# Optimization experiments

Hardware: AMD Instinct MI355X
Metric: run time of the kernel (lower is better)

## Reference

```python
import jax, jax.numpy as jnp
import numpy as np

STATE_DIM = 512
ACTION_FEAT_DIM = 64
HIDDEN = 256


def setup_inputs() -> dict:
    key = jax.random.key(0)
    ks = jax.random.split(key, 8)
    B, K = 256, 1000
    state_embed = jax.random.normal(ks[0], (B, STATE_DIM), dtype=jnp.float32)
    action_feats = jax.random.normal(ks[1], (B, K, ACTION_FEAT_DIM), dtype=jnp.float32)
    s = 0.05
    W1 = jax.random.normal(ks[2], (STATE_DIM + ACTION_FEAT_DIM, HIDDEN), dtype=jnp.float32) * s
    b1 = jnp.zeros((HIDDEN,), dtype=jnp.float32)
    W2 = jax.random.normal(ks[3], (HIDDEN, HIDDEN // 2), dtype=jnp.float32) * s
    b2 = jnp.zeros((HIDDEN // 2,), dtype=jnp.float32)
    W3 = jax.random.normal(ks[4], (HIDDEN // 2, 1), dtype=jnp.float32) * s
    b3 = jnp.zeros((1,), dtype=jnp.float32)
    return {"state_embed": state_embed, "action_feats": action_feats,
            "W1": W1, "b1": b1, "W2": W2, "b2": b2, "W3": W3, "b3": b3}


def reference(state_embed, action_feats, W1, b1, W2, b2, W3, b3):
    # Faithful math: concat([state broadcast to K, action_feats]) -> Linear/ReLU x2 -> Linear(1)
    # Efficient form: split W1 rows so state part is computed once per batch row.
    W1_s = W1[:STATE_DIM]            # [state_dim, hidden]
    W1_a = W1[STATE_DIM:]            # [action_feat_dim, hidden]
    h_state = state_embed @ W1_s     # [B, hidden]
    h = jax.nn.relu(jnp.einsum('bkf,fh->bkh', action_feats, W1_a) + h_state[:, None, :] + b1)
    h = jax.nn.relu(jnp.einsum('bkh,hg->bkg', h, W2) + b2)
    logits = (jnp.einsum('bkg,go->bko', h, W3) + b3)[..., 0]  # [B, K]
    return logits
```

## Files before the change

kernel.cpp:

```cpp
#include <hip/hip_runtime.h>

typedef _Float16 f16;
typedef f16 f16x4 __attribute__((ext_vector_type(4)));
typedef f16 f16x8 __attribute__((ext_vector_type(8)));
typedef float f32x4 __attribute__((ext_vector_type(4)));


#define AF_STRIDE 64
#define H1_STRIDE 256

__global__ __launch_bounds__(256) void prep_kernel(const float* __restrict__ W1,
                                                   const float* __restrict__ W2,
                                                   const float* __restrict__ state,
                                                   const float* __restrict__ b1,
                                                   f16* __restrict__ pw1at,
                                                   f16* __restrict__ pw2,
                                                   float* __restrict__ hstate) {
    __shared__ float srow[512];
    int blk = blockIdx.x;
    int tid = threadIdx.x;
    if (blk < 24) {
        int idx = blk * 256 + tid;
        int F = idx >> 6;
        int L = idx & 63;
        int q = L >> 4, c = L & 15;
        f16x8 v;
        if (F < 32) {
            int mt = F >> 1, kt = F & 1;
            #pragma unroll
            for (int j = 0; j < 8; ++j) {
                int f = kt * 32 + q * 8 + j;
                v[j] = (f16)W1[(size_t)(512 + f) * 256 + mt * 16 + c];
            }
            *(f16x8*)(pw1at + ((size_t)F * 64 + L) * 8) = v;
        } else {
            int F2 = F - 32;
            int nt = F2 >> 3, kt = F2 & 7;
            #pragma unroll
            for (int j = 0; j < 8; ++j) {
                int k = kt * 32 + q * 8 + j;
                v[j] = (f16)W2[(size_t)k * 128 + nt * 16 + c];
            }
            *(f16x8*)(pw2 + ((size_t)F2 * 64 + L) * 8) = v;
        }
    } else {
        int b = blk - 24;
        srow[tid] = state[(size_t)b * 512 + tid];
        srow[tid + 256] = state[(size_t)b * 512 + 256 + tid];
        __syncthreads();
        float a0 = 0.f, a1 = 0.f;
        #pragma unroll 8
        for (int f = 0; f < 512; f += 2) {
            a0 = fmaf(srow[f],     W1[(size_t)f * 256 + tid],       a0);
            a1 = fmaf(srow[f + 1], W1[(size_t)(f + 1) * 256 + tid], a1);
        }
        hstate[(size_t)b * 256 + tid] = a0 + a1 + b1[tid];
    }
}

__global__ __launch_bounds__(256, 4) void fused_kernel(const float* __restrict__ afeat,
                                                       const float* __restrict__ hstate,
                                                       const f16* __restrict__ pw1at,
                                                       const f16* __restrict__ pw2,
                                                       const float* __restrict__ b2,
                                                       const float* __restrict__ W3,
                                                       const float* __restrict__ b3,
                                                       float* __restrict__ out) {
    __shared__ __align__(16) char smem[(64 * AF_STRIDE + 64 * H1_STRIDE) * 2];
    f16* afs = (f16*)smem;
    f16* h1s = (f16*)(smem + 64 * AF_STRIDE * 2);
    float* lds3 = (float*)smem;

    int tid = threadIdx.x;
    int w = tid >> 6;
    int L = tid & 63;
    int q = L >> 4, c = L & 15;
    int r0 = blockIdx.x * 64;

    f16x8 a1f[4][2];
    #pragma unroll
    for (int i = 0; i < 4; ++i)
        #pragma unroll
        for (int kt = 0; kt < 2; ++kt)
            a1f[i][kt] = *(const f16x8*)(pw1at + ((size_t)((4 * w + i) * 2 + kt) * 64 + L) * 8);

    #pragma unroll
    for (int i = 0; i < 2; ++i) {
        int id = i * 256 + tid;
        int row = id >> 3, c32 = id & 7;
        const float* p = afeat + (size_t)(r0 + row) * 64 + c32 * 8;
        f32x4 lo = *(const f32x4*)p;
        f32x4 hi = *(const f32x4*)(p + 4);
        f16x8 v;
        v[0] = (f16)lo[0]; v[1] = (f16)lo[1]; v[2] = (f16)lo[2]; v[3] = (f16)lo[3];
        v[4] = (f16)hi[0]; v[5] = (f16)hi[1]; v[6] = (f16)hi[2]; v[7] = (f16)hi[3];
        *(f16x8*)(afs + row * AF_STRIDE + ((c32 * 8) ^ ((row & 7) << 3))) = v;
    }

    float b3v = b3[0];
    float b2v[2], w3v[2];
    #pragma unroll
    for (int ntl = 0; ntl < 2; ++ntl) {
        int col = (w * 2 + ntl) * 16 + c;
        b2v[ntl] = b2[col];
        w3v[ntl] = W3[col];
    }
    __syncthreads();

    int b0i = r0 / 1000;
    int boundary = (b0i + 1) * 1000;
    int b1i = b0i < 255 ? b0i + 1 : 255;
    int sx = (c & 7) << 3;

    f16x8 bf[4][2];
    #pragma unroll
    for (int nt = 0; nt < 4; ++nt)
        #pragma unroll
        for (int kt = 0; kt < 2; ++kt)
            bf[nt][kt] = *(const f16x8*)(afs + (nt * 16 + c) * AF_STRIDE + ((kt * 32 + q * 8) ^ sx));

    #pragma unroll
    for (int i = 0; i < 4; ++i) {
        f32x4 acc[4];
        #pragma unroll
        for (int nt = 0; nt < 4; ++nt) {
            acc[nt] = (f32x4){0.f, 0.f, 0.f, 0.f};
            #pragma unroll
            for (int kt = 0; kt < 2; ++kt)
                acc[nt] = __builtin_amdgcn_mfma_f32_16x16x32_f16(
                    a1f[i][kt], bf[nt][kt], acc[nt], 0, 0, 0);
        }
        int hbase = (4 * w + i) * 16 + q * 4;
        f32x4 hsA = *(const f32x4*)(hstate + (size_t)b0i * 256 + hbase);
        f32x4 hsB = *(const f32x4*)(hstate + (size_t)b1i * 256 + hbase);
        #pragma unroll
        for (int nt = 0; nt < 4; ++nt) {
            bool sel = (r0 + nt * 16 + c) >= boundary;
            f16x4 hv;
            #pragma unroll
            for (int reg = 0; reg < 4; ++reg) {
                float v = acc[nt][reg] + (sel ? hsB[reg] : hsA[reg]);
                v = v > 0.f ? v : 0.f;
                hv[reg] = (f16)v;
            }
            *(f16x4*)(h1s + (nt * 16 + c) * H1_STRIDE + (hbase ^ sx)) = hv;
        }
    }
    __syncthreads();

    f32x4 acc2[4][2];
    #pragma unroll
    for (int rb = 0; rb < 4; ++rb) {
        acc2[rb][0] = (f32x4){0.f, 0.f, 0.f, 0.f};
        acc2[rb][1] = (f32x4){0.f, 0.f, 0.f, 0.f};
    }
    #pragma unroll
    for (int kt = 0; kt < 8; ++kt) {
        f16x8 a2[4];
        #pragma unroll
        for (int rb = 0; rb < 4; ++rb)
            a2[rb] = *(const f16x8*)(h1s + (rb * 16 + c) * H1_STRIDE + ((kt * 32 + q * 8) ^ sx));
        #pragma unroll
        for (int ntl = 0; ntl < 2; ++ntl) {
            f16x8 bfr = *(const f16x8*)(pw2 + ((size_t)((w * 2 + ntl) * 8 + kt) * 64 + L) * 8);
            #pragma unroll
            for (int rb = 0; rb < 4; ++rb)
                acc2[rb][ntl] = __builtin_amdgcn_mfma_f32_16x16x32_f16(
                    a2[rb], bfr, acc2[rb][ntl], 0, 0, 0);
        }
    }

    float p[16];
    #pragma unroll
    for (int rb = 0; rb < 4; ++rb)
        #pragma unroll
        for (int reg = 0; reg < 4; ++reg) {
            float v0 = acc2[rb][0][reg] + b2v[0]; v0 = v0 > 0.f ? v0 : 0.f;
            float v1 = acc2[rb][1][reg] + b2v[1]; v1 = v1 > 0.f ? v1 : 0.f;
            p[rb * 4 + reg] = fmaf(v0, w3v[0], v1 * w3v[1]);
        }
    float s0[8];
    #pragma unroll
    for (int i = 0; i < 8; ++i) {
        float send = (c & 1) ? p[2 * i] : p[2 * i + 1];
        float keep = (c & 1) ? p[2 * i + 1] : p[2 * i];
        s0[i] = keep + __shfl_xor(send, 1);
    }
    float s1[4];
    #pragma unroll
    for (int i = 0; i < 4; ++i) {
        float send = (c & 2) ? s0[2 * i] : s0[2 * i + 1];
        float keep = (c & 2) ? s0[2 * i + 1] : s0[2 * i];
        s1[i] = keep + __shfl_xor(send, 2);
    }
    float s2[2];
    #pragma unroll
    for (int i = 0; i < 2; ++i) {
        float send = (c & 4) ? s1[2 * i] : s1[2 * i + 1];
        float keep = (c & 4) ? s1[2 * i + 1] : s1[2 * i];
        s2[i] = keep + __shfl_xor(send, 4);
    }
    float send3 = (c & 8) ? s2[0] : s2[1];
    float keep3 = (c & 8) ? s2[1] : s2[0];
    float s3 = keep3 + __shfl_xor(send3, 8);
    int m = (c >> 2) * 16 + q * 4 + (c & 3);
    lds3[m * 6 + w] = s3;
    __syncthreads();

    if (tid < 64) {
        const float* pm = lds3 + tid * 6;
        out[r0 + tid] = pm[0] + pm[1] + pm[2] + pm[3] + b3v;
    }
}

extern "C" void kernel_launch(void* const* d_in, const int* in_sizes, int n_in,
                              void* d_out, int out_size, void* d_ws, size_t ws_size,
                              hipStream_t stream) {
    const float* state = (const float*)d_in[0];
    const float* afeat = (const float*)d_in[1];
    const float* W1    = (const float*)d_in[2];
    const float* b1    = (const float*)d_in[3];
    const float* W2    = (const float*)d_in[4];
    const float* b2    = (const float*)d_in[5];
    const float* W3    = (const float*)d_in[6];
    const float* b3    = (const float*)d_in[7];
    float* out = (float*)d_out;

    float* hstate = (float*)d_ws;
    f16* pw1at = (f16*)((char*)d_ws + 65536 * sizeof(float));
    f16* pw2   = pw1at + 16384;

    prep_kernel<<<280, 256, 0, stream>>>(W1, W2, state, b1, pw1at, pw2, hstate);
    fused_kernel<<<4000, 256, 0, stream>>>(afeat, hstate, pw1at, pw2, b2, W3, b3, out);
}
```

Before: 137.0 us.

## Swap layer-2 MFMA operands, prefetch W2 fragments, simplify logit reduction

Layer 2 now passes the W2 fragment as the A operand and the hidden activations as B, so each lane's accumulator holds four hidden columns for one row. This lets the W3 dot product run mostly in registers, followed by two cross-lane shuffles instead of a four-stage shuffle tree. W2 fragments are double-buffered one k-step ahead, hstate loads are hoisted before the layer-1 MFMAs, and the prep loop's unroll factor goes from 8 to 16. The aim is to hide global load latency and cut shuffle and ALU work in the epilogue, at the cost of more registers under the 4-blocks-per-CU launch bound.

```diff
diff --git a/kernel.cpp b/kernel.cpp
--- a/kernel.cpp
+++ b/kernel.cpp
@@ -49,7 +49,7 @@
         srow[tid + 256] = state[(size_t)b * 512 + 256 + tid];
         __syncthreads();
         float a0 = 0.f, a1 = 0.f;
-        #pragma unroll 8
+        #pragma unroll 16
         for (int f = 0; f < 512; f += 2) {
             a0 = fmaf(srow[f],     W1[(size_t)f * 256 + tid],       a0);
             a1 = fmaf(srow[f + 1], W1[(size_t)(f + 1) * 256 + tid], a1);
@@ -97,19 +97,21 @@
         *(f16x8*)(afs + row * AF_STRIDE + ((c32 * 8) ^ ((row & 7) << 3))) = v;
     }
 
-    float b3v = b3[0];
-    float b2v[2], w3v[2];
-    #pragma unroll
-    for (int ntl = 0; ntl < 2; ++ntl) {
-        int col = (w * 2 + ntl) * 16 + c;
-        b2v[ntl] = b2[col];
-        w3v[ntl] = W3[col];
-    }
-    __syncthreads();
-
     int b0i = r0 / 1000;
     int boundary = (b0i + 1) * 1000;
     int b1i = b0i < 255 ? b0i + 1 : 255;
+
+    f32x4 hsva[4], hsvb[4];
+    #pragma unroll
+    for (int i = 0; i < 4; ++i) {
+        int hbase = (4 * w + i) * 16 + q * 4;
+        hsva[i] = *(const f32x4*)(hstate + (size_t)b0i * 256 + hbase);
+        hsvb[i] = *(const f32x4*)(hstate + (size_t)b1i * 256 + hbase);
+    }
+
+    float b3v = b3[0];
+    __syncthreads();
+
     int sx = (c & 7) << 3;
 
     f16x8 bf[4][2];
@@ -131,15 +133,13 @@
                     a1f[i][kt], bf[nt][kt], acc[nt], 0, 0, 0);
         }
         int hbase = (4 * w + i) * 16 + q * 4;
-        f32x4 hsA = *(const f32x4*)(hstate + (size_t)b0i * 256 + hbase);
-        f32x4 hsB = *(const f32x4*)(hstate + (size_t)b1i * 256 + hbase);
         #pragma unroll
         for (int nt = 0; nt < 4; ++nt) {
             bool sel = (r0 + nt * 16 + c) >= boundary;
             f16x4 hv;
             #pragma unroll
             for (int reg = 0; reg < 4; ++reg) {
-                float v = acc[nt][reg] + (sel ? hsB[reg] : hsA[reg]);
+                float v = acc[nt][reg] + (sel ? hsvb[i][reg] : hsva[i][reg]);
                 v = v > 0.f ? v : 0.f;
                 hv[reg] = (f16)v;
             }
@@ -147,6 +147,14 @@
         }
     }
     __syncthreads();
+
+    f32x4 b2v[2], w3v[2];
+    #pragma unroll
+    for (int gti = 0; gti < 2; ++gti) {
+        int gb = (2 * w + gti) * 16 + q * 4;
+        b2v[gti] = *(const f32x4*)(b2 + gb);
+        w3v[gti] = *(const f32x4*)(W3 + gb);
+    }
 
     f32x4 acc2[4][2];
     #pragma unroll
@@ -154,57 +162,56 @@
         acc2[rb][0] = (f32x4){0.f, 0.f, 0.f, 0.f};
         acc2[rb][1] = (f32x4){0.f, 0.f, 0.f, 0.f};
     }
+
+    f16x8 pwf[2][2];
+    #pragma unroll
+    for (int gti = 0; gti < 2; ++gti)
+        pwf[0][gti] = *(const f16x8*)(pw2 + ((size_t)((2 * w + gti) * 8 + 0) * 64 + L) * 8);
+
     #pragma unroll
     for (int kt = 0; kt < 8; ++kt) {
+        if (kt < 7) {
+            #pragma unroll
+            for (int gti = 0; gti < 2; ++gti)
+                pwf[(kt + 1) & 1][gti] =
+                    *(const f16x8*)(pw2 + ((size_t)((2 * w + gti) * 8 + kt + 1) * 64 + L) * 8);
+        }
         f16x8 a2[4];
         #pragma unroll
         for (int rb = 0; rb < 4; ++rb)
             a2[rb] = *(const f16x8*)(h1s + (rb * 16 + c) * H1_STRIDE + ((kt * 32 + q * 8) ^ sx));
         #pragma unroll
-        for (int ntl = 0; ntl < 2; ++ntl) {
-            f16x8 bfr = *(const f16x8*)(pw2 + ((size_t)((w * 2 + ntl) * 8 + kt) * 64 + L) * 8);
+        for (int gti = 0; gti < 2; ++gti)
             #pragma unroll
             for (int rb = 0; rb < 4; ++rb)
-                acc2[rb][ntl] = __builtin_amdgcn_mfma_f32_16x16x32_f16(
-                    a2[rb], bfr, acc2[rb][ntl], 0, 0, 0);
-        }
-    }
-
-    float p[16];
-    #pragma unroll
-    for (int rb = 0; rb < 4; ++rb)
-        #pragma unroll
-        for (int reg = 0; reg < 4; ++reg) {
-            float v0 = acc2[rb][0][reg] + b2v[0]; v0 = v0 > 0.f ? v0 : 0.f;
-            float v1 = acc2[rb][1][reg] + b2v[1]; v1 = v1 > 0.f ? v1 : 0.f;
-            p[rb * 4 + reg] = fmaf(v0, w3v[0], v1 * w3v[1]);
-        }
-    float s0[8];
-    #pragma unroll
-    for (int i = 0; i < 8; ++i) {
-        float send = (c & 1) ? p[2 * i] : p[2 * i + 1];
-        float keep = (c & 1) ? p[2 * i + 1] : p[2 * i];
-        s0[i] = keep + __shfl_xor(send, 1);
-    }
-    float s1[4];
-    #pragma unroll
-    for (int i = 0; i < 4; ++i) {
-        float send = (c & 2) ? s0[2 * i] : s0[2 * i + 1];
-        float keep = (c & 2) ? s0[2 * i + 1] : s0[2 * i];
-        s1[i] = keep + __shfl_xor(send, 2);
-    }
-    float s2[2];
-    #pragma unroll
-    for (int i = 0; i < 2; ++i) {
-        float send = (c & 4) ? s1[2 * i] : s1[2 * i + 1];
-        float keep = (c & 4) ? s1[2 * i + 1] : s1[2 * i];
-        s2[i] = keep + __shfl_xor(send, 4);
-    }
-    float send3 = (c & 8) ? s2[0] : s2[1];
-    float keep3 = (c & 8) ? s2[1] : s2[0];
-    float s3 = keep3 + __shfl_xor(send3, 8);
-    int m = (c >> 2) * 16 + q * 4 + (c & 3);
-    lds3[m * 6 + w] = s3;
+                acc2[rb][gti] = __builtin_amdgcn_mfma_f32_16x16x32_f16(
+                    pwf[kt & 1][gti], a2[rb], acc2[rb][gti], 0, 0, 0);
+    }
+
+    float pa[4];
+    #pragma unroll
+    for (int rb = 0; rb < 4; ++rb) {
+        float s = 0.f;
+        #pragma unroll
+        for (int gti = 0; gti < 2; ++gti)
+            #pragma unroll
+            for (int reg = 0; reg < 4; ++reg) {
+                float v = acc2[rb][gti][reg] + b2v[gti][reg];
+                v = v > 0.f ? v : 0.f;
+                s = fmaf(v, w3v[gti][reg], s);
+            }
+        pa[rb] = s;
+    }
+    #pragma unroll
+    for (int rb = 0; rb < 4; ++rb) {
+        pa[rb] += __shfl_xor(pa[rb], 16);
+        pa[rb] += __shfl_xor(pa[rb], 32);
+    }
+    if (L < 16) {
+        #pragma unroll
+        for (int rb = 0; rb < 4; ++rb)
+            lds3[(rb * 16 + L) * 6 + w] = pa[rb];
+    }
     __syncthreads();
 
     if (tid < 64) {
```

Result: faster. 133.6 us (-2.5%).
